# Optimization experiments

Measured on AMD Instinct MI355X. Metric: run time of the kernel, lower is better.

The kernel has to match this reference:

```python
import jax, jax.numpy as jnp
import numpy as np

B, S, D, H = 4, 2048, 1024, 16
HS = D // H          # head size 64
DF = 4 * D           # ffn hidden 4096
EPS = 1e-5


def _layer_norm(x, g, b):
    mu = jnp.mean(x, axis=-1, keepdims=True)
    var = jnp.var(x, axis=-1, keepdims=True)
    return (x - mu) * jax.lax.rsqrt(var + EPS) * g + b


def setup_inputs() -> dict:
    key = jax.random.key(0)
    ks = jax.random.split(key, 12)
    s_d = 1.0 / np.sqrt(D)
    s_f = 1.0 / np.sqrt(DF)
    return {
        "x": jax.random.normal(ks[0], (B, S, D), jnp.float32),
        # per-head q/k/v projections, batched over heads: [H, D, HS]
        "wq": jax.random.uniform(ks[1], (H, D, HS), jnp.float32, -s_d, s_d),
        "wk": jax.random.uniform(ks[2], (H, D, HS), jnp.float32, -s_d, s_d),
        "wv": jax.random.uniform(ks[3], (H, D, HS), jnp.float32, -s_d, s_d),
        "proj_w": jax.random.uniform(ks[4], (D, D), jnp.float32, -s_d, s_d),
        "proj_b": jax.random.uniform(ks[5], (D,), jnp.float32, -s_d, s_d),
        "ff1_w": jax.random.uniform(ks[6], (D, DF), jnp.float32, -s_d, s_d),
        "ff1_b": jax.random.uniform(ks[7], (DF,), jnp.float32, -s_d, s_d),
        "ff2_w": jax.random.uniform(ks[8], (DF, D), jnp.float32, -s_f, s_f),
        "ff2_b": jax.random.uniform(ks[9], (D,), jnp.float32, -s_f, s_f),
        "ln1_g": jnp.ones((D,), jnp.float32),
        "ln1_b": jnp.zeros((D,), jnp.float32),
        "ln2_g": jnp.ones((D,), jnp.float32),
        "ln2_b": jnp.zeros((D,), jnp.float32),
    }


def reference(x, wq, wk, wv, proj_w, proj_b, ff1_w, ff1_b, ff2_w, ff2_b,
              ln1_g, ln1_b, ln2_g, ln2_b):
    # --- multi-head causal self-attention on ln1(x), all heads batched ---
    h = _layer_norm(x, ln1_g, ln1_b)                      # [B,S,D]
    q = jnp.einsum("bsd,hde->bhse", h, wq)                # [B,H,S,HS]
    k = jnp.einsum("bsd,hde->bhse", h, wk)
    v = jnp.einsum("bsd,hde->bhse", h, wv)
    scale = HS ** -0.5
    scores = jnp.einsum("bhse,bhte->bhst", q, k) * scale  # [B,H,S,S]
    causal = jnp.tril(jnp.ones((S, S), bool))
    scores = jnp.where(causal, scores, jnp.finfo(scores.dtype).min)
    att = jax.nn.softmax(scores, axis=-1)
    o = jnp.einsum("bhst,bhte->bhse", att, v)             # [B,H,S,HS]
    o = o.transpose(0, 2, 1, 3).reshape(B, S, D)          # concat heads
    sa = o @ proj_w + proj_b
    x = x + sa
    # --- FFN on ln2(x) ---
    h2 = _layer_norm(x, ln2_g, ln2_b)
    ff = jax.nn.relu(h2 @ ff1_w + ff1_b) @ ff2_w + ff2_b
    return x + ff
```

## Files before the change

### kernel.cpp

```cpp
#include <hip/hip_runtime.h>
#include <hip/hip_bf16.h>

#define BB 4
#define SS 2048
#define DD 1024
#define HH 16
#define HSZ 64
#define DFF 4096

typedef short short8 __attribute__((ext_vector_type(8)));
typedef float f32x4 __attribute__((ext_vector_type(4)));
typedef unsigned short us4 __attribute__((ext_vector_type(4)));

#define AS1 __attribute__((address_space(1)))
#define AS3 __attribute__((address_space(3)))

__device__ __forceinline__ unsigned short f2bf(float f) {
    return __bfloat16_as_ushort(__float2bfloat16(f));
}

__global__ __launch_bounds__(256) void pack_qkv_kernel(
    const float* __restrict__ wq, const float* __restrict__ wk,
    const float* __restrict__ wv, __hip_bfloat16* __restrict__ out)
{
    int id = blockIdx.x * 256 + threadIdx.x;
    int n = id >> 10;
    int k = id & 1023;
    int sel = n >> 10;
    int hn = n & 1023;
    int h = hn >> 6, e = hn & 63;
    const float* src = (sel == 0) ? wq : (sel == 1) ? wk : wv;
    out[id] = __float2bfloat16(src[(size_t)h * (DD * HSZ) + (size_t)k * HSZ + e]);
}

__global__ __launch_bounds__(256) void pack_T_kernel(
    const float* __restrict__ in, __hip_bfloat16* __restrict__ out, int K, int N)
{
    int id = blockIdx.x * 256 + threadIdx.x;
    int n = id / K;
    int k = id - n * K;
    out[id] = __float2bfloat16(in[(size_t)k * N + n]);
}

__global__ __launch_bounds__(256) void ln_kernel(
    const float* __restrict__ x, const float* __restrict__ g,
    const float* __restrict__ b, __hip_bfloat16* __restrict__ out)
{
    int row = blockIdx.x;
    int t = threadIdx.x;
    const float4* xr = (const float4*)(x + (size_t)row * DD);
    float4 v = xr[t];
    float s = v.x + v.y + v.z + v.w;
    float ss = v.x * v.x + v.y * v.y + v.z * v.z + v.w * v.w;
    #pragma unroll
    for (int off = 32; off; off >>= 1) {
        s += __shfl_xor(s, off, 64);
        ss += __shfl_xor(ss, off, 64);
    }
    __shared__ float red[8];
    int w = t >> 6, lane = t & 63;
    if (lane == 0) { red[w] = s; red[4 + w] = ss; }
    __syncthreads();
    s = red[0] + red[1] + red[2] + red[3];
    ss = red[4] + red[5] + red[6] + red[7];
    float mu = s * (1.f / DD);
    float var = ss * (1.f / DD) - mu * mu;
    float rs = rsqrtf(var + 1e-5f);
    float4 gv = ((const float4*)g)[t];
    float4 bv = ((const float4*)b)[t];
    ushort4 pk = make_ushort4(
        f2bf((v.x - mu) * rs * gv.x + bv.x),
        f2bf((v.y - mu) * rs * gv.y + bv.y),
        f2bf((v.z - mu) * rs * gv.z + bv.z),
        f2bf((v.w - mu) * rs * gv.w + bv.w));
    *(ushort4*)((unsigned short*)out + (size_t)row * DD + t * 4) = pk;
}

template<int BN, bool BIAS, bool RELU, bool RES, bool OUTF32>
__global__ __launch_bounds__(512) void gemm_kernel(
    const __hip_bfloat16* __restrict__ A, const __hip_bfloat16* __restrict__ BT,
    const float* __restrict__ bias, const float* __restrict__ res,
    void* __restrict__ Cout, int M, int N, int K, int nbx)
{
    constexpr int WN = (BN == 256) ? 4 : 2;
    constexpr int MREP = (BN == 256) ? 8 : 4;
    constexpr int BLOADS = BN / 64;
    __shared__ uint4 As[2][2048];
    __shared__ uint4 Bs[2][BN * 8];

    const int t = threadIdx.x;
    const int lane = t & 63, w = t >> 6;
    const int lr = lane & 15, g = lane >> 4;
    const int nwg = gridDim.x;
    const int cpx = nwg >> 3;
    const int wg = blockIdx.x;
    const int swz = (wg & 7) * cpx + (wg >> 3);
    const int bx = swz % nbx, by = swz / nbx;
    const int row0 = by * 256, col0 = bx * BN;
    const int wr = (w / WN) * (MREP * 16), wc = (w % WN) * 64;

    f32x4 acc[MREP][4] = {};
    const int NT = K >> 6;

    auto stage = [&](int buf, int k0) {
        #pragma unroll
        for (int j = 0; j < 4; ++j) {
            int s = j * 512 + t;
            int r = s >> 3;
            int kb = (s & 7) ^ (r & 7);
            const __hip_bfloat16* src = A + (size_t)(row0 + r) * K + k0 + kb * 8;
            __builtin_amdgcn_global_load_lds((const AS1 void*)src,
                (AS3 void*)(&As[buf][j * 512 + (t & ~63)]), 16, 0, 0);
        }
        #pragma unroll
        for (int j = 0; j < BLOADS; ++j) {
            int s = j * 512 + t;
            int r = s >> 3;
            int kb = (s & 7) ^ (r & 7);
            const __hip_bfloat16* src = BT + (size_t)(col0 + r) * K + k0 + kb * 8;
            __builtin_amdgcn_global_load_lds((const AS1 void*)src,
                (AS3 void*)(&Bs[buf][j * 512 + (t & ~63)]), 16, 0, 0);
        }
    };

    auto compute = [&](int buf) {
        short8 bf[4][2];
        #pragma unroll
        for (int n = 0; n < 4; ++n) {
            int c = wc + n * 16 + lr;
            #pragma unroll
            for (int kk = 0; kk < 2; ++kk)
                bf[n][kk] = *(const short8*)&Bs[buf][c * 8 + ((kk * 4 + g) ^ (c & 7))];
        }
        #pragma unroll
        for (int ph = 0; ph < MREP / 2; ++ph) {
            short8 af[2][2];
            #pragma unroll
            for (int m2 = 0; m2 < 2; ++m2) {
                int r = wr + ph * 32 + m2 * 16 + lr;
                #pragma unroll
                for (int kk = 0; kk < 2; ++kk)
                    af[m2][kk] = *(const short8*)&As[buf][r * 8 + ((kk * 4 + g) ^ (r & 7))];
            }
            __builtin_amdgcn_s_setprio(1);
            #pragma unroll
            for (int m2 = 0; m2 < 2; ++m2)
                #pragma unroll
                for (int n = 0; n < 4; ++n)
                    #pragma unroll
                    for (int kk = 0; kk < 2; ++kk)
                        acc[ph * 2 + m2][n] = __builtin_amdgcn_mfma_f32_16x16x32_bf16(
                            af[m2][kk], bf[n][kk], acc[ph * 2 + m2][n], 0, 0, 0);
            __builtin_amdgcn_s_setprio(0);
        }
    };

    stage(0, 0);
    int cur = 0;
    for (int tt = 0; tt < NT - 1; ++tt) {
        stage(cur ^ 1, (tt + 1) * 64);
        if constexpr (BN == 256) asm volatile("s_waitcnt vmcnt(8)" ::: "memory");
        else                     asm volatile("s_waitcnt vmcnt(6)" ::: "memory");
        __builtin_amdgcn_s_barrier();
        compute(cur);
        __builtin_amdgcn_sched_barrier(0);
        __builtin_amdgcn_s_barrier();
        cur ^= 1;
    }
    asm volatile("s_waitcnt vmcnt(0)" ::: "memory");
    __builtin_amdgcn_s_barrier();
    compute(cur);

    #pragma unroll
    for (int mi = 0; mi < MREP; ++mi) {
        #pragma unroll
        for (int j = 0; j < 4; ++j) {
            int rr = row0 + wr + mi * 16 + g * 4 + j;
            #pragma unroll
            for (int n = 0; n < 4; ++n) {
                int cc = col0 + wc + n * 16 + lr;
                float vv = acc[mi][n][j];
                if (BIAS) vv += bias[cc];
                if (RELU) vv = fmaxf(vv, 0.f);
                if (RES) vv += res[(size_t)rr * N + cc];
                if (OUTF32) ((float*)Cout)[(size_t)rr * N + cc] = vv;
                else ((__hip_bfloat16*)Cout)[(size_t)rr * N + cc] = __float2bfloat16(vv);
            }
        }
    }
}

__device__ __forceinline__ void stage_kv(
    const unsigned short* __restrict__ qkvu, size_t rowbase, int h, int kv0, int tl,
    unsigned short* __restrict__ Kb, unsigned short* __restrict__ Vb)
{
    {
        int kv = tl >> 2, c = tl & 3;
        const unsigned short* src = qkvu + rowbase + (size_t)(kv0 + kv) * 3072 + DD + h * HSZ + c * 16;
        uint4 v0 = *(const uint4*)src;
        uint4 v1 = *(const uint4*)(src + 8);
        int sw = kv & 7;
        *(uint4*)&Kb[kv * 64 + ((2 * c) ^ sw) * 8] = v0;
        *(uint4*)&Kb[kv * 64 + ((2 * c + 1) ^ sw) * 8] = v1;
    }
    {
        int bkv = ((tl >> 6) << 2) | (tl & 3);
        int bd = (tl >> 2) & 15;
        const unsigned short* src = qkvu + rowbase + (size_t)(kv0 + bkv * 4) * 3072 + 2 * DD + h * HSZ + bd * 4;
        us4 r0 = *(const us4*)src;
        us4 r1 = *(const us4*)(src + 3072);
        us4 r2 = *(const us4*)(src + 2 * 3072);
        us4 r3 = *(const us4*)(src + 3 * 3072);
        #pragma unroll
        for (int cc = 0; cc < 4; ++cc) {
            int d = bd * 4 + cc;
            us4 wv = { r0[cc], r1[cc], r2[cc], r3[cc] };
            *(us4*)&Vb[d * 64 + (((bkv >> 1) ^ (d & 7)) * 8) + (bkv & 1) * 4] = wv;
        }
    }
}

__device__ __forceinline__ void flash_tile(
    const unsigned short* __restrict__ Kb, const unsigned short* __restrict__ Vb,
    unsigned short* __restrict__ Pw, const short8* qfc, int qgc, int kv0, int q, int g,
    float& m_run, float& l_run, f32x4* oacc)
{
    f32x4 st[4] = {};
    __builtin_amdgcn_s_setprio(1);
    #pragma unroll
    for (int tt = 0; tt < 4; ++tt) {
        #pragma unroll
        for (int kk = 0; kk < 2; ++kk) {
            short8 kf = *(const short8*)&Kb[(tt * 16 + q) * 64 + ((4 * kk + g) ^ (q & 7)) * 8];
            st[tt] = __builtin_amdgcn_mfma_f32_16x16x32_bf16(kf, qfc[kk], st[tt], 0, 0, 0);
        }
    }
    __builtin_amdgcn_s_setprio(0);

    float mt = -1e30f;
    #pragma unroll
    for (int tt = 0; tt < 4; ++tt)
        #pragma unroll
        for (int j = 0; j < 4; ++j) {
            float s = st[tt][j] * 0.125f;
            int kvg = kv0 + tt * 16 + g * 4 + j;
            s = (kvg <= qgc) ? s : -1e30f;
            st[tt][j] = s;
            mt = fmaxf(mt, s);
        }
    mt = fmaxf(mt, __shfl_xor(mt, 16, 64));
    mt = fmaxf(mt, __shfl_xor(mt, 32, 64));
    float m_new = fmaxf(m_run, mt);
    float corr = __expf(m_run - m_new);
    float lsum = 0.f;
    #pragma unroll
    for (int tt = 0; tt < 4; ++tt)
        #pragma unroll
        for (int j = 0; j < 4; ++j) {
            float p = __expf(st[tt][j] - m_new);
            st[tt][j] = p;
            lsum += p;
        }
    lsum += __shfl_xor(lsum, 16, 64);
    lsum += __shfl_xor(lsum, 32, 64);
    l_run = l_run * corr + lsum;
    m_run = m_new;

    #pragma unroll
    for (int tt = 0; tt < 4; ++tt) {
        unsigned int lo = ((unsigned int)f2bf(st[tt][1]) << 16) | (unsigned int)f2bf(st[tt][0]);
        unsigned int hi = ((unsigned int)f2bf(st[tt][3]) << 16) | (unsigned int)f2bf(st[tt][2]);
        uint2 pk = make_uint2(lo, hi);
        *(uint2*)&Pw[q * 64 + ((2 * tt + (g >> 1)) ^ (q & 7)) * 8 + (g & 1) * 4] = pk;
    }

    #pragma unroll
    for (int j = 0; j < 4; ++j) {
        float cj = __shfl(corr, g * 4 + j, 64);
        #pragma unroll
        for (int dn = 0; dn < 4; ++dn)
            oacc[dn][j] *= cj;
    }

    __builtin_amdgcn_s_setprio(1);
    #pragma unroll
    for (int kk = 0; kk < 2; ++kk) {
        short8 pf = *(const short8*)&Pw[q * 64 + ((4 * kk + g) ^ (q & 7)) * 8];
        #pragma unroll
        for (int dn = 0; dn < 4; ++dn) {
            short8 vf = *(const short8*)&Vb[(dn * 16 + q) * 64 + ((4 * kk + g) ^ (q & 7)) * 8];
            oacc[dn] = __builtin_amdgcn_mfma_f32_16x16x32_bf16(pf, vf, oacc[dn], 0, 0, 0);
        }
    }
    __builtin_amdgcn_s_setprio(0);
}

__global__ __launch_bounds__(512) void attn_kernel(
    const __hip_bfloat16* __restrict__ qkv, __hip_bfloat16* __restrict__ o)
{
    __shared__ unsigned short K_lds[2][64 * 64];
    __shared__ unsigned short Vt_lds[2][64 * 64];
    __shared__ unsigned short P_lds[8 * 1024];

    const int t = threadIdx.x;
    const int lane = t & 63, w = t >> 6;
    const int grp = w >> 2, wq4 = w & 3, tl = t & 255;
    const int q = lane & 15, g = lane >> 4;
    const int pq = blockIdx.x & 15;
    const int h = (blockIdx.x >> 4) & 15;
    const int b = blockIdx.x >> 8;
    const int qtA = pq, qtB = 31 - pq;
    const int qt1 = grp ? qtB : qtA;
    const unsigned short* qkvu = (const unsigned short*)qkv;
    const size_t rowbase = (size_t)(b * SS) * 3072;
    unsigned short* Kb = K_lds[grp];
    unsigned short* Vb = Vt_lds[grp];
    unsigned short* Pw = &P_lds[w * 1024];
    unsigned short* op = (unsigned short*)o;

    int qgc = qt1 * 64 + wq4 * 16 + q;
    short8 qfc[2];
    #pragma unroll
    for (int kk = 0; kk < 2; ++kk)
        qfc[kk] = *(const short8*)(qkvu + rowbase + (size_t)qgc * 3072 + h * HSZ + kk * 32 + g * 8);

    f32x4 oacc[4] = {};
    float m_run = -1e30f, l_run = 0.f;

    for (int it = 0; it <= pq; ++it) {
        __syncthreads();
        stage_kv(qkvu, rowbase, h, it * 64, tl, Kb, Vb);
        __syncthreads();
        flash_tile(Kb, Vb, Pw, qfc, qgc, it * 64, q, g, m_run, l_run, oacc);
    }

    if (grp == 0) {
        #pragma unroll
        for (int j = 0; j < 4; ++j) {
            float lj = __shfl(l_run, g * 4 + j, 64);
            float inv = 1.f / lj;
            int orow = qtA * 64 + wq4 * 16 + g * 4 + j;
            #pragma unroll
            for (int dn = 0; dn < 4; ++dn)
                op[(size_t)(b * SS + orow) * DD + h * HSZ + dn * 16 + q] = f2bf(oacc[dn][j] * inv);
        }
        qgc = qtB * 64 + wq4 * 16 + q;
        #pragma unroll
        for (int kk = 0; kk < 2; ++kk)
            qfc[kk] = *(const short8*)(qkvu + rowbase + (size_t)qgc * 3072 + h * HSZ + kk * 32 + g * 8);
        m_run = -1e30f; l_run = 0.f;
        #pragma unroll
        for (int dn = 0; dn < 4; ++dn) oacc[dn] = f32x4{0.f, 0.f, 0.f, 0.f};
    }

    for (int it2 = 0; it2 < 16 - pq; ++it2) {
        int tile = grp ? (pq + 1 + it2) : (16 + it2);
        bool active = grp ? (tile <= 15) : true;
        __syncthreads();
        if (active) stage_kv(qkvu, rowbase, h, tile * 64, tl, Kb, Vb);
        __syncthreads();
        if (active) flash_tile(Kb, Vb, Pw, qfc, qgc, tile * 64, q, g, m_run, l_run, oacc);
    }

    __syncthreads();
    float* obuf = (float*)K_lds;
    float* mlbuf = (float*)P_lds;
    if (grp == 0) {
        #pragma unroll
        for (int dn = 0; dn < 4; ++dn)
            #pragma unroll
            for (int j = 0; j < 4; ++j)
                obuf[wq4 * 1024 + lane * 16 + dn * 4 + j] = oacc[dn][j];
        if (g == 0) { mlbuf[wq4 * 32 + q] = m_run; mlbuf[wq4 * 32 + 16 + q] = l_run; }
    }
    __syncthreads();
    if (grp == 1) {
        float mA = mlbuf[wq4 * 32 + q];
        float lA = mlbuf[wq4 * 32 + 16 + q];
        float mM = fmaxf(m_run, mA);
        float sB = __expf(m_run - mM);
        float sA = __expf(mA - mM);
        float lM = l_run * sB + lA * sA;
        #pragma unroll
        for (int j = 0; j < 4; ++j) {
            float sBj = __shfl(sB, g * 4 + j, 64);
            float sAj = __shfl(sA, g * 4 + j, 64);
            float lMj = __shfl(lM, g * 4 + j, 64);
            float inv = 1.f / lMj;
            int orow = qtB * 64 + wq4 * 16 + g * 4 + j;
            #pragma unroll
            for (int dn = 0; dn < 4; ++dn) {
                float oA = obuf[wq4 * 1024 + lane * 16 + dn * 4 + j];
                float vv = (oacc[dn][j] * sBj + oA * sAj) * inv;
                op[(size_t)(b * SS + orow) * DD + h * HSZ + dn * 16 + q] = f2bf(vv);
            }
        }
    }
}

extern "C" void kernel_launch(void* const* d_in, const int* in_sizes, int n_in,
                              void* d_out, int out_size, void* d_ws, size_t ws_size,
                              hipStream_t stream)
{
    const float* x      = (const float*)d_in[0];
    const float* wq     = (const float*)d_in[1];
    const float* wk     = (const float*)d_in[2];
    const float* wv     = (const float*)d_in[3];
    const float* proj_w = (const float*)d_in[4];
    const float* proj_b = (const float*)d_in[5];
    const float* ff1_w  = (const float*)d_in[6];
    const float* ff1_b  = (const float*)d_in[7];
    const float* ff2_w  = (const float*)d_in[8];
    const float* ff2_b  = (const float*)d_in[9];
    const float* ln1_g  = (const float*)d_in[10];
    const float* ln1_b  = (const float*)d_in[11];
    const float* ln2_g  = (const float*)d_in[12];
    const float* ln2_b  = (const float*)d_in[13];
    float* out = (float*)d_out;

    char* ws = (char*)d_ws;
    const size_t MB = 1ull << 20;
    __hip_bfloat16* h     = (__hip_bfloat16*)(ws);
    __hip_bfloat16* qkv   = (__hip_bfloat16*)(ws + 16 * MB);
    __hip_bfloat16* obuf  = (__hip_bfloat16*)(ws + 64 * MB);
    float*          x1    = (float*)(ws + 80 * MB);
    __hip_bfloat16* wqkvT = (__hip_bfloat16*)(ws + 112 * MB);
    __hip_bfloat16* projT = (__hip_bfloat16*)(ws + 118 * MB);
    __hip_bfloat16* ff1T  = (__hip_bfloat16*)(ws + 120 * MB);
    __hip_bfloat16* ff2T  = (__hip_bfloat16*)(ws + 128 * MB);
    __hip_bfloat16* f1    = (__hip_bfloat16*)(ws + 16 * MB);

    const int ROWS = BB * SS;

    pack_qkv_kernel<<<(3 * DD * DD) / 256, 256, 0, stream>>>(wq, wk, wv, wqkvT);
    pack_T_kernel<<<(DD * DD) / 256, 256, 0, stream>>>(proj_w, projT, DD, DD);
    pack_T_kernel<<<(DD * DFF) / 256, 256, 0, stream>>>(ff1_w, ff1T, DD, DFF);
    pack_T_kernel<<<(DFF * DD) / 256, 256, 0, stream>>>(ff2_w, ff2T, DFF, DD);

    ln_kernel<<<ROWS, 256, 0, stream>>>(x, ln1_g, ln1_b, h);
    gemm_kernel<256, false, false, false, false><<<(ROWS / 256) * (3 * DD / 256), 512, 0, stream>>>(
        h, wqkvT, nullptr, nullptr, qkv, ROWS, 3 * DD, DD, 3 * DD / 256);
    attn_kernel<<<BB * HH * 16, 512, 0, stream>>>(qkv, obuf);
    gemm_kernel<128, true, false, true, true><<<(ROWS / 256) * (DD / 128), 512, 0, stream>>>(
        obuf, projT, proj_b, x, x1, ROWS, DD, DD, DD / 128);
    ln_kernel<<<ROWS, 256, 0, stream>>>(x1, ln2_g, ln2_b, h);
    gemm_kernel<256, true, true, false, false><<<(ROWS / 256) * (DFF / 256), 512, 0, stream>>>(
        h, ff1T, ff1_b, nullptr, f1, ROWS, DFF, DD, DFF / 256);
    gemm_kernel<128, true, false, true, true><<<(ROWS / 256) * (DD / 128), 512, 0, stream>>>(
        f1, ff2T, ff2_b, x1, out, ROWS, DD, DFF, DD / 128);
}
```

Baseline: 441.9 us.

## Tile weight-pack transposes through LDS and restructure GEMM into half-tile pipelined phases

Measured after the change: 418.3 us. -5.3%, faster.

```diff
diff --git a/kernel.cpp b/kernel.cpp
--- a/kernel.cpp
+++ b/kernel.cpp
@@ -23,23 +23,41 @@
     const float* __restrict__ wq, const float* __restrict__ wk,
     const float* __restrict__ wv, __hip_bfloat16* __restrict__ out)
 {
-    int id = blockIdx.x * 256 + threadIdx.x;
-    int n = id >> 10;
-    int k = id & 1023;
-    int sel = n >> 10;
-    int hn = n & 1023;
-    int h = hn >> 6, e = hn & 63;
+    __shared__ float tile[64][65];
+    const int bid = blockIdx.x;
+    const int kt = bid & 15, hh = (bid >> 4) & 15, sel = bid >> 8;
     const float* src = (sel == 0) ? wq : (sel == 1) ? wk : wv;
-    out[id] = __float2bfloat16(src[(size_t)h * (DD * HSZ) + (size_t)k * HSZ + e]);
+    src += (size_t)hh * (DD * HSZ) + (size_t)kt * 64 * HSZ;
+    const int tx = threadIdx.x & 63, ty = threadIdx.x >> 6;
+    #pragma unroll
+    for (int r = 0; r < 64; r += 4)
+        tile[r + ty][tx] = src[(size_t)(r + ty) * HSZ + tx];
+    __syncthreads();
+    unsigned short* o = (unsigned short*)out + (size_t)(sel * DD + hh * 64) * DD + kt * 64;
+    #pragma unroll
+    for (int r = 0; r < 64; r += 4) {
+        int e = r + ty;
+        o[(size_t)e * DD + tx] = f2bf(tile[tx][e]);
+    }
 }
 
 __global__ __launch_bounds__(256) void pack_T_kernel(
     const float* __restrict__ in, __hip_bfloat16* __restrict__ out, int K, int N)
 {
-    int id = blockIdx.x * 256 + threadIdx.x;
-    int n = id / K;
-    int k = id - n * K;
-    out[id] = __float2bfloat16(in[(size_t)k * N + n]);
+    __shared__ float tile[64][65];
+    const int nb = N >> 6;
+    const int tn0 = (blockIdx.x % nb) << 6, tk0 = (blockIdx.x / nb) << 6;
+    const int tx = threadIdx.x & 63, ty = threadIdx.x >> 6;
+    #pragma unroll
+    for (int r = 0; r < 64; r += 4)
+        tile[r + ty][tx] = in[(size_t)(tk0 + r + ty) * N + tn0 + tx];
+    __syncthreads();
+    unsigned short* o = (unsigned short*)out;
+    #pragma unroll
+    for (int r = 0; r < 64; r += 4) {
+        int n = r + ty;
+        o[(size_t)(tn0 + n) * K + tk0 + tx] = f2bf(tile[tx][n]);
+    }
 }
 
 __global__ __launch_bounds__(256) void ln_kernel(
@@ -82,14 +100,14 @@
     const float* __restrict__ bias, const float* __restrict__ res,
     void* __restrict__ Cout, int M, int N, int K, int nbx)
 {
-    constexpr int WN = (BN == 256) ? 4 : 2;
-    constexpr int MREP = (BN == 256) ? 8 : 4;
-    constexpr int BLOADS = BN / 64;
-    __shared__ uint4 As[2][2048];
-    __shared__ uint4 Bs[2][BN * 8];
-
-    const int t = threadIdx.x;
-    const int lane = t & 63, w = t >> 6;
+    constexpr int NB = BN / 128;
+    constexpr int NREP = BN / 64;
+    __shared__ uint4 Ah[2][2][1024];
+    __shared__ uint4 Bh[2][NB][1024];
+
+    const int tid = threadIdx.x;
+    const int lane = tid & 63;
+    const int w = tid >> 6;
     const int lr = lane & 15, g = lane >> 4;
     const int nwg = gridDim.x;
     const int cpx = nwg >> 3;
@@ -97,97 +115,130 @@
     const int swz = (wg & 7) * cpx + (wg >> 3);
     const int bx = swz % nbx, by = swz / nbx;
     const int row0 = by * 256, col0 = bx * BN;
-    const int wr = (w / WN) * (MREP * 16), wc = (w % WN) * 64;
-
-    f32x4 acc[MREP][4] = {};
+    const int wm = w >> 2, wn = w & 3;
     const int NT = K >> 6;
 
-    auto stage = [&](int buf, int k0) {
-        #pragma unroll
-        for (int j = 0; j < 4; ++j) {
-            int s = j * 512 + t;
+    f32x4 acc0[4][NREP] = {};
+    f32x4 acc1[4][NREP] = {};
+    short8 bfr[NREP][2];
+
+    auto stageA = [&](int buf, int half, int t) {
+        const int k0 = t * 64;
+        #pragma unroll
+        for (int j = 0; j < 2; ++j) {
+            int s = j * 512 + tid;
             int r = s >> 3;
-            int kb = (s & 7) ^ (r & 7);
-            const __hip_bfloat16* src = A + (size_t)(row0 + r) * K + k0 + kb * 8;
+            int c = (s & 7) ^ (r & 7);
+            const __hip_bfloat16* src = A + (size_t)(row0 + half * 128 + r) * K + k0 + c * 8;
             __builtin_amdgcn_global_load_lds((const AS1 void*)src,
-                (AS3 void*)(&As[buf][j * 512 + (t & ~63)]), 16, 0, 0);
-        }
-        #pragma unroll
-        for (int j = 0; j < BLOADS; ++j) {
-            int s = j * 512 + t;
+                (AS3 void*)(&Ah[buf][half][j * 512 + (tid & ~63)]), 16, 0, 0);
+        }
+    };
+    auto stageB = [&](int buf, int half, int t) {
+        const int k0 = t * 64;
+        #pragma unroll
+        for (int j = 0; j < 2; ++j) {
+            int s = j * 512 + tid;
             int r = s >> 3;
-            int kb = (s & 7) ^ (r & 7);
-            const __hip_bfloat16* src = BT + (size_t)(col0 + r) * K + k0 + kb * 8;
+            int c = (s & 7) ^ (r & 7);
+            const __hip_bfloat16* src = BT + (size_t)(col0 + half * 128 + r) * K + k0 + c * 8;
             __builtin_amdgcn_global_load_lds((const AS1 void*)src,
-                (AS3 void*)(&Bs[buf][j * 512 + (t & ~63)]), 16, 0, 0);
+                (AS3 void*)(&Bh[buf][half][j * 512 + (tid & ~63)]), 16, 0, 0);
         }
     };
-
-    auto compute = [&](int buf) {
-        short8 bf[4][2];
-        #pragma unroll
-        for (int n = 0; n < 4; ++n) {
-            int c = wc + n * 16 + lr;
+    auto loadB = [&](int buf) {
+        const int hb = (NB == 2) ? (wn >> 1) : 0;
+        const int cb = (NB == 2) ? ((wn & 1) * 64) : (wn * 32);
+        #pragma unroll
+        for (int n = 0; n < NREP; ++n) {
+            int c = cb + n * 16 + lr;
             #pragma unroll
             for (int kk = 0; kk < 2; ++kk)
-                bf[n][kk] = *(const short8*)&Bs[buf][c * 8 + ((kk * 4 + g) ^ (c & 7))];
-        }
-        #pragma unroll
-        for (int ph = 0; ph < MREP / 2; ++ph) {
-            short8 af[2][2];
-            #pragma unroll
-            for (int m2 = 0; m2 < 2; ++m2) {
-                int r = wr + ph * 32 + m2 * 16 + lr;
+                bfr[n][kk] = *(const short8*)&Bh[buf][hb][c * 8 + ((kk * 4 + g) ^ (c & 7))];
+        }
+    };
+    auto phase = [&](auto& acc, int buf, int mh) {
+        short8 af[4][2];
+        #pragma unroll
+        for (int mi = 0; mi < 4; ++mi) {
+            int r = wm * 64 + mi * 16 + lr;
+            #pragma unroll
+            for (int kk = 0; kk < 2; ++kk)
+                af[mi][kk] = *(const short8*)&Ah[buf][mh][r * 8 + ((kk * 4 + g) ^ (r & 7))];
+        }
+        asm volatile("s_waitcnt lgkmcnt(0)" ::: "memory");
+        __builtin_amdgcn_sched_barrier(0);
+        __builtin_amdgcn_s_setprio(1);
+        #pragma unroll
+        for (int mi = 0; mi < 4; ++mi)
+            #pragma unroll
+            for (int n = 0; n < NREP; ++n)
                 #pragma unroll
                 for (int kk = 0; kk < 2; ++kk)
-                    af[m2][kk] = *(const short8*)&As[buf][r * 8 + ((kk * 4 + g) ^ (r & 7))];
+                    acc[mi][n] = __builtin_amdgcn_mfma_f32_16x16x32_bf16(
+                        af[mi][kk], bfr[n][kk], acc[mi][n], 0, 0, 0);
+        __builtin_amdgcn_s_setprio(0);
+    };
+
+    stageA(0, 0, 0);
+    stageB(0, 0, 0);
+    if constexpr (NB == 2) stageB(0, 1, 0);
+    stageA(0, 1, 0);
+    stageA(1, 0, 1);
+    if constexpr (NB == 2) stageB(1, 0, 1);
+
+    for (int t = 0; t < NT; ++t) {
+        const int buf = t & 1;
+        if (t < NT - 1) {
+            if constexpr (NB == 2) asm volatile("s_waitcnt vmcnt(4)" ::: "memory");
+            else                   asm volatile("s_waitcnt vmcnt(2)" ::: "memory");
+        } else {
+            asm volatile("s_waitcnt vmcnt(0)" ::: "memory");
+        }
+        __builtin_amdgcn_s_barrier();
+        __builtin_amdgcn_sched_barrier(0);
+        if (t + 1 < NT) {
+            if constexpr (NB == 2) { stageB(buf ^ 1, 1, t + 1); stageA(buf ^ 1, 1, t + 1); }
+            else                   { stageB(buf ^ 1, 0, t + 1); stageA(buf ^ 1, 1, t + 1); }
+        }
+        loadB(buf);
+        phase(acc0, buf, 0);
+        if (t < NT - 1) {
+            if constexpr (NB == 2) asm volatile("s_waitcnt vmcnt(8)" ::: "memory");
+            else                   asm volatile("s_waitcnt vmcnt(6)" ::: "memory");
+        } else {
+            asm volatile("s_waitcnt vmcnt(0)" ::: "memory");
+        }
+        __builtin_amdgcn_s_barrier();
+        __builtin_amdgcn_sched_barrier(0);
+        if (t + 2 < NT) {
+            stageA(buf, 0, t + 2);
+            if constexpr (NB == 2) stageB(buf, 0, t + 2);
+        }
+        phase(acc1, buf, 1);
+    }
+
+    auto store = [&](auto& acc, int mh) {
+        #pragma unroll
+        for (int mi = 0; mi < 4; ++mi) {
+            #pragma unroll
+            for (int j = 0; j < 4; ++j) {
+                int rr = row0 + mh * 128 + wm * 64 + mi * 16 + g * 4 + j;
+                #pragma unroll
+                for (int n = 0; n < NREP; ++n) {
+                    int cc = col0 + wn * (NREP * 16) + n * 16 + lr;
+                    float vv = acc[mi][n][j];
+                    if (BIAS) vv += bias[cc];
+                    if (RELU) vv = fmaxf(vv, 0.f);
+                    if (RES) vv += res[(size_t)rr * N + cc];
+                    if (OUTF32) ((float*)Cout)[(size_t)rr * N + cc] = vv;
+                    else ((__hip_bfloat16*)Cout)[(size_t)rr * N + cc] = __float2bfloat16(vv);
+                }
             }
-            __builtin_amdgcn_s_setprio(1);
-            #pragma unroll
-            for (int m2 = 0; m2 < 2; ++m2)
-                #pragma unroll
-                for (int n = 0; n < 4; ++n)
-                    #pragma unroll
-                    for (int kk = 0; kk < 2; ++kk)
-                        acc[ph * 2 + m2][n] = __builtin_amdgcn_mfma_f32_16x16x32_bf16(
-                            af[m2][kk], bf[n][kk], acc[ph * 2 + m2][n], 0, 0, 0);
-            __builtin_amdgcn_s_setprio(0);
         }
     };
-
-    stage(0, 0);
-    int cur = 0;
-    for (int tt = 0; tt < NT - 1; ++tt) {
-        stage(cur ^ 1, (tt + 1) * 64);
-        if constexpr (BN == 256) asm volatile("s_waitcnt vmcnt(8)" ::: "memory");
-        else                     asm volatile("s_waitcnt vmcnt(6)" ::: "memory");
-        __builtin_amdgcn_s_barrier();
-        compute(cur);
-        __builtin_amdgcn_sched_barrier(0);
-        __builtin_amdgcn_s_barrier();
-        cur ^= 1;
-    }
-    asm volatile("s_waitcnt vmcnt(0)" ::: "memory");
-    __builtin_amdgcn_s_barrier();
-    compute(cur);
-
-    #pragma unroll
-    for (int mi = 0; mi < MREP; ++mi) {
-        #pragma unroll
-        for (int j = 0; j < 4; ++j) {
-            int rr = row0 + wr + mi * 16 + g * 4 + j;
-            #pragma unroll
-            for (int n = 0; n < 4; ++n) {
-                int cc = col0 + wc + n * 16 + lr;
-                float vv = acc[mi][n][j];
-                if (BIAS) vv += bias[cc];
-                if (RELU) vv = fmaxf(vv, 0.f);
-                if (RES) vv += res[(size_t)rr * N + cc];
-                if (OUTF32) ((float*)Cout)[(size_t)rr * N + cc] = vv;
-                else ((__hip_bfloat16*)Cout)[(size_t)rr * N + cc] = __float2bfloat16(vv);
-            }
-        }
-    }
+    store(acc0, 0);
+    store(acc1, 1);
 }
 
 __device__ __forceinline__ void stage_kv(
@@ -432,14 +483,14 @@
 
     const int ROWS = BB * SS;
 
-    pack_qkv_kernel<<<(3 * DD * DD) / 256, 256, 0, stream>>>(wq, wk, wv, wqkvT);
-    pack_T_kernel<<<(DD * DD) / 256, 256, 0, stream>>>(proj_w, projT, DD, DD);
-    pack_T_kernel<<<(DD * DFF) / 256, 256, 0, stream>>>(ff1_w, ff1T, DD, DFF);
-    pack_T_kernel<<<(DFF * DD) / 256, 256, 0, stream>>>(ff2_w, ff2T, DFF, DD);
+    pack_qkv_kernel<<<768, 256, 0, stream>>>(wq, wk, wv, wqkvT);
+    pack_T_kernel<<<(DD / 64) * (DD / 64), 256, 0, stream>>>(proj_w, projT, DD, DD);
+    pack_T_kernel<<<(DFF / 64) * (DD / 64), 256, 0, stream>>>(ff1_w, ff1T, DD, DFF);
+    pack_T_kernel<<<(DD / 64) * (DFF / 64), 256, 0, stream>>>(ff2_w, ff2T, DFF, DD);
 
     ln_kernel<<<ROWS, 256, 0, stream>>>(x, ln1_g, ln1_b, h);
-    gemm_kernel<256, false, false, false, false><<<(ROWS / 256) * (3 * DD / 256), 512, 0, stream>>>(
-        h, wqkvT, nullptr, nullptr, qkv, ROWS, 3 * DD, DD, 3 * DD / 256);
+    gemm_kernel<128, false, false, false, false><<<(ROWS / 256) * (3 * DD / 128), 512, 0, stream>>>(
+        h, wqkvT, nullptr, nullptr, qkv, ROWS, 3 * DD, DD, 3 * DD / 128);
     attn_kernel<<<BB * HH * 16, 512, 0, stream>>>(qkv, obuf);
     gemm_kernel<128, true, false, true, true><<<(ROWS / 256) * (DD / 128), 512, 0, stream>>>(
         obuf, projT, proj_b, x, x1, ROWS, DD, DD, DD / 128);
```
